# Kernel optimization log

Hardware: AMD Instinct MI355X
Metric: run time of the kernel (lower is better)

## Reference

```python
import jax, jax.numpy as jnp
import numpy as np

C = 32
KSHAPE = (C, C, 3, 3)  # (C_out, C_in, kH, kW)
BN_EPS = 1e-5


def _binary_act(x):
    # forward: sign(x); backward: identity clipped to |x|<1 (STE)
    xc = jnp.clip(x, -1.0, 1.0)
    return jax.lax.stop_gradient(jnp.sign(x) - xc) + xc


def _binarize_weight(w_flat, shape):
    w = w_flat.reshape(shape)
    scale = jax.lax.stop_gradient(jnp.mean(jnp.abs(w)))  # global scalar scale, detached
    wc = jnp.clip(w, -1.0, 1.0)
    # forward: scale*sign(w); backward flows through clamp(w,-1,1)
    return jax.lax.stop_gradient(scale * jnp.sign(w) - wc) + wc


def _bi_conv_bn(x, w_flat, gamma, beta, stride):
    xb = _binary_act(x)
    w = _binarize_weight(w_flat, KSHAPE)
    y = jax.lax.conv_general_dilated(
        xb, w, window_strides=(stride, stride), padding=[(1, 1), (1, 1)],
        dimension_numbers=('NCHW', 'OIHW', 'NCHW'))
    # BatchNorm2d in training mode (batch stats, biased variance)
    m = jnp.mean(y, axis=(0, 2, 3), keepdims=True)
    v = jnp.mean((y - m) ** 2, axis=(0, 2, 3), keepdims=True)
    yhat = (y - m) * jax.lax.rsqrt(v + BN_EPS)
    return gamma.reshape(1, -1, 1, 1) * yhat + beta.reshape(1, -1, 1, 1)


def setup_inputs() -> dict:
    key = jax.random.key(0)
    k1, k2, k3 = jax.random.split(key, 3)
    return {
        'x': jax.random.normal(k1, (32, C, 160, 160), dtype=jnp.float32),
        'w1': jax.random.normal(k2, (C * C * 9, 1), dtype=jnp.float32) * 0.05,
        'gamma1': jnp.ones((C,), dtype=jnp.float32),
        'beta1': jnp.zeros((C,), dtype=jnp.float32),
        'w2': jax.random.normal(k3, (C * C * 9, 1), dtype=jnp.float32) * 0.05,
        'gamma2': jnp.ones((C,), dtype=jnp.float32),
        'beta2': jnp.zeros((C,), dtype=jnp.float32),
    }


def reference(x, w1, gamma1, beta1, w2, gamma2, beta2):
    # bireal residual block, stride=1 => skip_op is Identity
    inner = _bi_conv_bn(x, w1, gamma1, beta1, 1) + x
    out = _bi_conv_bn(inner, w2, gamma2, beta2, 1) + inner
    return out
```

## Files before the change

### kernel.cpp

```cpp
#include <hip/hip_runtime.h>
#include <stdint.h>

#define NIMG 32
#define CH 32
#define HH 160
#define WW 160
#define HWL (HH*WW)
#define PRS 164
#define PHH 162
#define PIMG (PHH*PRS)
#define NPIX (NIMG*HWL)
#define HALO_WORDS 968

#define OFF_P     0
#define OFF_P2    3400704
#define OFF_INNER (OFF_P2 + 3400704)
#define OFF_WP    (OFF_INNER + 52428800)
#define OFF_CORR  (OFF_WP + 2304)
#define OFF_SC    (OFF_CORR + 2304)
#define OFF_SB    (OFF_SC + 128)

struct StatLine {
  int s1; int pad0; unsigned long long s2; char pad[112];
};

__device__ __forceinline__ unsigned short f2bf(float f) {
  unsigned u = __float_as_uint(f);
  u += 0x7fffu + ((u >> 16) & 1u);
  return (unsigned short)(u >> 16);
}
__device__ __forceinline__ float bf2f(unsigned short u) {
  return __uint_as_float((uint32_t)u << 16);
}

__device__ __forceinline__ void conv4(const uint32_t r[3][6], const uint32_t* wsh,
                                      int co, int& a0, int& a1, int& a2, int& a3)
{
  a0 = a1 = a2 = a3 = 0;
  #pragma unroll
  for (int dy = 0; dy < 3; ++dy) {
    #pragma unroll
    for (int dx = 0; dx < 3; ++dx) {
      uint32_t wvv = wsh[co * 9 + dy * 3 + dx];
      a0 += __popc(r[dy][0 + dx] ^ wvv);
      a1 += __popc(r[dy][1 + dx] ^ wvv);
      a2 += __popc(r[dy][2 + dx] ^ wvv);
      a3 += __popc(r[dy][3 + dx] ^ wvv);
    }
  }
}

__global__ __launch_bounds__(256, 2) void pack_prep(const float* __restrict__ x,
    const float* __restrict__ w1, const float* __restrict__ w2,
    uint32_t* __restrict__ P, uint32_t* __restrict__ P2, uint32_t* __restrict__ WP,
    int* __restrict__ CORR, float* __restrict__ SC, StatLine* __restrict__ SB)
{
  __shared__ float red[256];
  const int tid = threadIdx.x;
  const int b = blockIdx.x;

  if (b >= 1600) {
    if (b == 1842) {
      int* z = (int*)SB;
      for (int i = tid; i < 2048; i += 256) z[i] = 0;
      for (int cv = 0; cv < 2; ++cv) {
        const float* w = cv ? w2 : w1;
        float s = 0.f;
        for (int i = tid; i < 9216; i += 256) s += fabsf(w[i]);
        red[tid] = s;
        __syncthreads();
        for (int st = 128; st > 0; st >>= 1) {
          if (tid < st) red[tid] += red[tid + st];
          __syncthreads();
        }
        if (tid == 0) SC[cv] = red[0] / 9216.0f;
        for (int i = tid; i < 288; i += 256) {
          int co = i / 9, t = i - co * 9;
          uint32_t bw = 0;
          for (int ci = 0; ci < 32; ++ci)
            bw |= (w[(co * 32 + ci) * 9 + t] > 0.0f) ? (1u << ci) : 0u;
          WP[cv * 288 + i] = bw;
        }
        __syncthreads();
        for (int i = tid; i < 288; i += 256) {
          int cls = i / 32, co = i - cls * 32;
          int hc = cls / 3, wc = cls - hc * 3;
          int corr = 0;
          for (int t = 0; t < 9; ++t) {
            int dy = t / 3 - 1, dx = t % 3 - 1;
            bool inval = (hc == 0 && dy == -1) || (hc == 2 && dy == 1) ||
                         (wc == 0 && dx == -1) || (wc == 2 && dx == 1);
            if (inval) corr += 32 - 2 * __popc(WP[cv * 288 + co * 9 + t]);
          }
          CORR[cv * 288 + cls * 32 + co] = corr;
        }
        __syncthreads();
      }
    } else {
      int k = (b - 1600) * 256 + tid;
      uint32_t* buf = (k < 32 * HALO_WORDS) ? P : P2;
      int j = k % (32 * HALO_WORDS);
      int img = j / HALO_WORDS;
      int r = j - img * HALO_WORDS;
      int pr, pc;
      if (r < 164)      { pr = 0;   pc = r; }
      else if (r < 328) { pr = 161; pc = r - 164; }
      else {
        int k2 = r - 328;
        pr = 1 + (k2 >> 2);
        int q = k2 & 3;
        pc = (q == 0) ? 0 : (160 + q);
      }
      buf[img * PIMG + pr * PRS + pc] = 0;
    }
    return;
  }

  int g = b * 256 + tid;
  int grp = g >> 2;
  int k = g & 3;
  int p0 = grp * 8;
  int n = p0 / HWL;
  int i = p0 - n * HWL;
  const float* xb = x + (size_t)n * CH * HWL + i + (size_t)(k * 8) * HWL;
  float4 a0 = *reinterpret_cast<const float4*>(xb + 0 * HWL);
  float4 b0 = *reinterpret_cast<const float4*>(xb + 0 * HWL + 4);
  float4 a1 = *reinterpret_cast<const float4*>(xb + 1 * HWL);
  float4 b1 = *reinterpret_cast<const float4*>(xb + 1 * HWL + 4);
  float4 a2 = *reinterpret_cast<const float4*>(xb + 2 * HWL);
  float4 b2 = *reinterpret_cast<const float4*>(xb + 2 * HWL + 4);
  float4 a3 = *reinterpret_cast<const float4*>(xb + 3 * HWL);
  float4 b3 = *reinterpret_cast<const float4*>(xb + 3 * HWL + 4);
  float4 a4 = *reinterpret_cast<const float4*>(xb + 4 * HWL);
  float4 b4 = *reinterpret_cast<const float4*>(xb + 4 * HWL + 4);
  float4 a5 = *reinterpret_cast<const float4*>(xb + 5 * HWL);
  float4 b5 = *reinterpret_cast<const float4*>(xb + 5 * HWL + 4);
  float4 a6 = *reinterpret_cast<const float4*>(xb + 6 * HWL);
  float4 b6 = *reinterpret_cast<const float4*>(xb + 6 * HWL + 4);
  float4 a7 = *reinterpret_cast<const float4*>(xb + 7 * HWL);
  float4 b7 = *reinterpret_cast<const float4*>(xb + 7 * HWL + 4);

  uint32_t q0 = 0, q1 = 0, q2 = 0, q3 = 0, q4 = 0, q5 = 0, q6 = 0, q7 = 0;
  int c0 = k * 8;
  #define ACC(j, aj, bj)                                        \
    { uint32_t m = 1u << (c0 + j);                              \
      if (aj.x > 0.f) q0 |= m; if (aj.y > 0.f) q1 |= m;         \
      if (aj.z > 0.f) q2 |= m; if (aj.w > 0.f) q3 |= m;         \
      if (bj.x > 0.f) q4 |= m; if (bj.y > 0.f) q5 |= m;         \
      if (bj.z > 0.f) q6 |= m; if (bj.w > 0.f) q7 |= m; }
  ACC(0, a0, b0) ACC(1, a1, b1) ACC(2, a2, b2) ACC(3, a3, b3)
  ACC(4, a4, b4) ACC(5, a5, b5) ACC(6, a6, b6) ACC(7, a7, b7)
  #undef ACC

  q0 |= __shfl_xor(q0, 1); q1 |= __shfl_xor(q1, 1);
  q2 |= __shfl_xor(q2, 1); q3 |= __shfl_xor(q3, 1);
  q4 |= __shfl_xor(q4, 1); q5 |= __shfl_xor(q5, 1);
  q6 |= __shfl_xor(q6, 1); q7 |= __shfl_xor(q7, 1);
  q0 |= __shfl_xor(q0, 2); q1 |= __shfl_xor(q1, 2);
  q2 |= __shfl_xor(q2, 2); q3 |= __shfl_xor(q3, 2);
  q4 |= __shfl_xor(q4, 2); q5 |= __shfl_xor(q5, 2);
  q6 |= __shfl_xor(q6, 2); q7 |= __shfl_xor(q7, 2);

  int h = i / WW, w = i - (i / WW) * WW;
  uint32_t* pw = P + n * PIMG + (h + 1) * PRS + (w + 1);
  uint32_t wa = (k == 0) ? q0 : (k == 1) ? q1 : (k == 2) ? q2 : q3;
  uint32_t wb = (k == 0) ? q4 : (k == 1) ? q5 : (k == 2) ? q6 : q7;
  pw[k] = wa;
  pw[k + 4] = wb;
}

__global__ __launch_bounds__(256) void conv_stats(const uint32_t* __restrict__ P,
    const uint32_t* __restrict__ WP, const int* __restrict__ CORR,
    StatLine* __restrict__ sb)
{
  __shared__ uint32_t wsh[288];
  __shared__ int csh[288];
  __shared__ int ls1[32], ls2[32];
  const int tid = threadIdx.x;
  for (int i = tid; i < 288; i += 256) { wsh[i] = WP[i]; csh[i] = CORR[i]; }
  if (tid < 32) { ls1[tid] = 0; ls2[tid] = 0; }
  __syncthreads();

  int g = blockIdx.x * 256 + tid;
  int w4 = g % 40;
  int t1 = g / 40;
  int h = t1 % 160;
  int n = t1 / 160;

  const uint32_t* base = P + n * PIMG + h * PRS + w4 * 4;
  uint32_t r[3][6];
  #pragma unroll
  for (int dy = 0; dy < 3; ++dy) {
    uint4 a = *reinterpret_cast<const uint4*>(base + dy * PRS);
    uint2 bw = *reinterpret_cast<const uint2*>(base + dy * PRS + 4);
    r[dy][0] = a.x; r[dy][1] = a.y; r[dy][2] = a.z; r[dy][3] = a.w;
    r[dy][4] = bw.x; r[dy][5] = bw.y;
  }

  int rowc = (h == 0) ? 0 : ((h == 159) ? 6 : 3);
  int cls0  = rowc + ((w4 == 0) ? 0 : 1);
  int cls12 = rowc + 1;
  int cls3  = rowc + ((w4 == 39) ? 2 : 1);
  int lane = tid & 63;

  #pragma unroll
  for (int co = 0; co < 32; ++co) {
    int a0, a1, a2, a3;
    conv4(r, wsh, co, a0, a1, a2, a3);
    int d0 = 288 - 2 * a0 - csh[cls0 * 32 + co];
    int d1 = 288 - 2 * a1 - csh[cls12 * 32 + co];
    int d2 = 288 - 2 * a2 - csh[cls12 * 32 + co];
    int d3 = 288 - 2 * a3 - csh[cls3 * 32 + co];
    int ds = d0 + d1 + d2 + d3;
    int sq = d0 * d0 + d1 * d1 + d2 * d2 + d3 * d3;
    #pragma unroll
    for (int off = 32; off > 0; off >>= 1) {
      ds += __shfl_down(ds, off);
      sq += __shfl_down(sq, off);
    }
    if (lane == 0) { atomicAdd(&ls1[co], ds); atomicAdd(&ls2[co], sq); }
  }
  __syncthreads();
  if (tid < 32) {
    atomicAdd(&sb[tid].s1, ls1[tid]);
    atomicAdd(&sb[tid].s2, (unsigned long long)(long long)ls2[tid]);
  }
}

__global__ __launch_bounds__(256, 2) void conv_bn1(const uint32_t* __restrict__ P,
    const uint32_t* __restrict__ WP, const int* __restrict__ CORR,
    const float* __restrict__ x, const float* __restrict__ SCp,
    const StatLine* __restrict__ sb, const float* __restrict__ gamma,
    const float* __restrict__ beta, unsigned short* __restrict__ INNER,
    uint32_t* __restrict__ P2)
{
  __shared__ uint32_t wsh[288];
  __shared__ int csh[288];
  __shared__ float Ash[32], Bsh[32];
  const int tid = threadIdx.x;
  for (int i = tid; i < 288; i += 256) { wsh[i] = WP[i]; csh[i] = CORR[i]; }
  if (tid < 32) {
    double sc = (double)SCp[0];
    double m  = sc * (double)sb[tid].s1 / (double)NPIX;
    double ms = sc * sc * (double)(long long)sb[tid].s2 / (double)NPIX;
    float inv = (float)(1.0 / sqrt(ms - m * m + 1e-5));
    float gm = gamma[tid];
    Ash[tid] = gm * inv * (float)sc;
    Bsh[tid] = beta[tid] - gm * inv * (float)m;
  }
  __syncthreads();

  int g = blockIdx.x * 256 + tid;
  int w4 = g % 40;
  int t1 = g / 40;
  int h = t1 % 160;
  int n = t1 / 160;

  const uint32_t* base = P + n * PIMG + h * PRS + w4 * 4;
  uint32_t r[3][6];
  #pragma unroll
  for (int dy = 0; dy < 3; ++dy) {
    uint4 a = *reinterpret_cast<const uint4*>(base + dy * PRS);
    uint2 bw = *reinterpret_cast<const uint2*>(base + dy * PRS + 4);
    r[dy][0] = a.x; r[dy][1] = a.y; r[dy][2] = a.z; r[dy][3] = a.w;
    r[dy][4] = bw.x; r[dy][5] = bw.y;
  }
  int rowc = (h == 0) ? 0 : ((h == 159) ? 6 : 3);
  int cls0  = rowc + ((w4 == 0) ? 0 : 1);
  int cls12 = rowc + 1;
  int cls3  = rowc + ((w4 == 39) ? 2 : 1);

  int i = h * WW + w4 * 4;
  size_t pbase = (size_t)n * CH * HWL + i;

  float4 xv[32];
  #pragma unroll
  for (int j = 0; j < 32; ++j)
    xv[j] = *reinterpret_cast<const float4*>(x + pbase + (size_t)j * HWL);

  uint32_t bb0 = 0, bb1 = 0, bb2 = 0, bb3 = 0;
  #pragma unroll
  for (int co = 0; co < 32; ++co) {
    int a0, a1, a2, a3;
    conv4(r, wsh, co, a0, a1, a2, a3);
    int d0 = 288 - 2 * a0 - csh[cls0 * 32 + co];
    int d1 = 288 - 2 * a1 - csh[cls12 * 32 + co];
    int d2 = 288 - 2 * a2 - csh[cls12 * 32 + co];
    int d3 = 288 - 2 * a3 - csh[cls3 * 32 + co];
    float A = Ash[co], Bv = Bsh[co];
    float v0 = fmaf(A, (float)d0, Bv) + xv[co].x;
    float v1 = fmaf(A, (float)d1, Bv) + xv[co].y;
    float v2 = fmaf(A, (float)d2, Bv) + xv[co].z;
    float v3 = fmaf(A, (float)d3, Bv) + xv[co].w;
    ushort4 o; o.x = f2bf(v0); o.y = f2bf(v1); o.z = f2bf(v2); o.w = f2bf(v3);
    *reinterpret_cast<ushort4*>(INNER + pbase + (size_t)co * HWL) = o;
    uint32_t m = 1u << co;
    if (v0 > 0.f) bb0 |= m;
    if (v1 > 0.f) bb1 |= m;
    if (v2 > 0.f) bb2 |= m;
    if (v3 > 0.f) bb3 |= m;
  }
  uint32_t* pw = P2 + n * PIMG + (h + 1) * PRS + (w4 * 4 + 1);
  pw[0] = bb0; pw[1] = bb1; pw[2] = bb2; pw[3] = bb3;
}

__global__ __launch_bounds__(256, 2) void conv_bn2(const uint32_t* __restrict__ P2,
    const uint32_t* __restrict__ WP, const int* __restrict__ CORR,
    const unsigned short* __restrict__ INNER, const float* __restrict__ SCp,
    const StatLine* __restrict__ sb, const float* __restrict__ gamma,
    const float* __restrict__ beta, float* __restrict__ out)
{
  __shared__ uint32_t wsh[288];
  __shared__ int csh[288];
  __shared__ float Ash[32], Bsh[32];
  const int tid = threadIdx.x;
  for (int i = tid; i < 288; i += 256) { wsh[i] = WP[i]; csh[i] = CORR[i]; }
  if (tid < 32) {
    double sc = (double)SCp[0];
    double m  = sc * (double)sb[tid].s1 / (double)NPIX;
    double ms = sc * sc * (double)(long long)sb[tid].s2 / (double)NPIX;
    float inv = (float)(1.0 / sqrt(ms - m * m + 1e-5));
    float gm = gamma[tid];
    Ash[tid] = gm * inv * (float)sc;
    Bsh[tid] = beta[tid] - gm * inv * (float)m;
  }
  __syncthreads();

  int g = blockIdx.x * 256 + tid;
  int w4 = g % 40;
  int t1 = g / 40;
  int h = t1 % 160;
  int n = t1 / 160;

  const uint32_t* base = P2 + n * PIMG + h * PRS + w4 * 4;
  uint32_t r[3][6];
  #pragma unroll
  for (int dy = 0; dy < 3; ++dy) {
    uint4 a = *reinterpret_cast<const uint4*>(base + dy * PRS);
    uint2 bw = *reinterpret_cast<const uint2*>(base + dy * PRS + 4);
    r[dy][0] = a.x; r[dy][1] = a.y; r[dy][2] = a.z; r[dy][3] = a.w;
    r[dy][4] = bw.x; r[dy][5] = bw.y;
  }
  int rowc = (h == 0) ? 0 : ((h == 159) ? 6 : 3);
  int cls0  = rowc + ((w4 == 0) ? 0 : 1);
  int cls12 = rowc + 1;
  int cls3  = rowc + ((w4 == 39) ? 2 : 1);

  int i = h * WW + w4 * 4;
  size_t pbase = (size_t)n * CH * HWL + i;

  ushort4 iv[32];
  #pragma unroll
  for (int j = 0; j < 32; ++j)
    iv[j] = *reinterpret_cast<const ushort4*>(INNER + pbase + (size_t)j * HWL);

  #pragma unroll
  for (int co = 0; co < 32; ++co) {
    int a0, a1, a2, a3;
    conv4(r, wsh, co, a0, a1, a2, a3);
    int d0 = 288 - 2 * a0 - csh[cls0 * 32 + co];
    int d1 = 288 - 2 * a1 - csh[cls12 * 32 + co];
    int d2 = 288 - 2 * a2 - csh[cls12 * 32 + co];
    int d3 = 288 - 2 * a3 - csh[cls3 * 32 + co];
    float A = Ash[co], Bv = Bsh[co];
    float4 o;
    o.x = fmaf(A, (float)d0, Bv) + bf2f(iv[co].x);
    o.y = fmaf(A, (float)d1, Bv) + bf2f(iv[co].y);
    o.z = fmaf(A, (float)d2, Bv) + bf2f(iv[co].z);
    o.w = fmaf(A, (float)d3, Bv) + bf2f(iv[co].w);
    *reinterpret_cast<float4*>(out + pbase + (size_t)co * HWL) = o;
  }
}

extern "C" void kernel_launch(void* const* d_in, const int* in_sizes, int n_in,
                              void* d_out, int out_size, void* d_ws, size_t ws_size,
                              hipStream_t stream)
{
  (void)in_sizes; (void)n_in; (void)out_size; (void)ws_size;
  const float* x  = (const float*)d_in[0];
  const float* w1 = (const float*)d_in[1];
  const float* g1 = (const float*)d_in[2];
  const float* b1 = (const float*)d_in[3];
  const float* w2 = (const float*)d_in[4];
  const float* g2 = (const float*)d_in[5];
  const float* b2 = (const float*)d_in[6];
  float* out = (float*)d_out;
  char* ws = (char*)d_ws;

  uint32_t*       P     = (uint32_t*)(ws + OFF_P);
  uint32_t*       P2    = (uint32_t*)(ws + OFF_P2);
  unsigned short* INNER = (unsigned short*)(ws + OFF_INNER);
  uint32_t*       WP    = (uint32_t*)(ws + OFF_WP);
  int*            CORR  = (int*)(ws + OFF_CORR);
  float*          SC    = (float*)(ws + OFF_SC);
  StatLine*       SB    = (StatLine*)(ws + OFF_SB);

  pack_prep<<<1843, 256, 0, stream>>>(x, w1, w2, P, P2, WP, CORR, SC, SB);
  conv_stats<<<800, 256, 0, stream>>>(P, WP, CORR, SB);
  conv_bn1<<<800, 256, 0, stream>>>(P, WP, CORR, x, SC, SB, g1, b1, INNER, P2);
  conv_stats<<<800, 256, 0, stream>>>(P2, WP + 288, CORR + 288, SB + 32);
  conv_bn2<<<800, 256, 0, stream>>>(P2, WP + 288, CORR + 288, INNER, SC + 1, SB + 32, g2, b2, out);
}
```

Measured before the change: 205.0 us.

## Stage input tiles into LDS via global_load_lds DMA for sign packing

```diff
diff --git a/kernel.cpp b/kernel.cpp
--- a/kernel.cpp
+++ b/kernel.cpp
@@ -24,6 +24,12 @@
   int s1; int pad0; unsigned long long s2; char pad[112];
 };
 
+#define AS1 __attribute__((address_space(1)))
+#define AS3 __attribute__((address_space(3)))
+__device__ __forceinline__ void dma16(const float* g, float* l) {
+  __builtin_amdgcn_global_load_lds((const AS1 void*)g, (AS3 void*)l, 16, 0, 0);
+}
+
 __device__ __forceinline__ unsigned short f2bf(float f) {
   unsigned u = __float_as_uint(f);
   u += 0x7fffu + ((u >> 16) & 1u);
@@ -50,12 +56,12 @@
   }
 }
 
-__global__ __launch_bounds__(256, 2) void pack_prep(const float* __restrict__ x,
+__global__ __launch_bounds__(256) void pack_prep(const float* __restrict__ x,
     const float* __restrict__ w1, const float* __restrict__ w2,
     uint32_t* __restrict__ P, uint32_t* __restrict__ P2, uint32_t* __restrict__ WP,
     int* __restrict__ CORR, float* __restrict__ SC, StatLine* __restrict__ SB)
 {
-  __shared__ float red[256];
+  __shared__ float lds[16384];
   const int tid = threadIdx.x;
   const int b = blockIdx.x;
 
@@ -63,10 +69,18 @@
     if (b == 1842) {
       int* z = (int*)SB;
       for (int i = tid; i < 2048; i += 256) z[i] = 0;
+      float* wl  = lds;
+      float* red = lds + 9216;
+      uint32_t* wpl = (uint32_t*)(lds + 9600);
       for (int cv = 0; cv < 2; ++cv) {
         const float* w = cv ? w2 : w1;
         float s = 0.f;
-        for (int i = tid; i < 9216; i += 256) s += fabsf(w[i]);
+        #pragma unroll
+        for (int j = 0; j < 9; ++j) {
+          float4 v = *reinterpret_cast<const float4*>(w + (j * 256 + tid) * 4);
+          *reinterpret_cast<float4*>(wl + (j * 256 + tid) * 4) = v;
+          s += fabsf(v.x) + fabsf(v.y) + fabsf(v.z) + fabsf(v.w);
+        }
         red[tid] = s;
         __syncthreads();
         for (int st = 128; st > 0; st >>= 1) {
@@ -78,8 +92,9 @@
           int co = i / 9, t = i - co * 9;
           uint32_t bw = 0;
           for (int ci = 0; ci < 32; ++ci)
-            bw |= (w[(co * 32 + ci) * 9 + t] > 0.0f) ? (1u << ci) : 0u;
+            bw |= (wl[(co * 32 + ci) * 9 + t] > 0.0f) ? (1u << ci) : 0u;
           WP[cv * 288 + i] = bw;
+          wpl[i] = bw;
         }
         __syncthreads();
         for (int i = tid; i < 288; i += 256) {
@@ -90,7 +105,7 @@
             int dy = t / 3 - 1, dx = t % 3 - 1;
             bool inval = (hc == 0 && dy == -1) || (hc == 2 && dy == 1) ||
                          (wc == 0 && dx == -1) || (wc == 2 && dx == 1);
-            if (inval) corr += 32 - 2 * __popc(WP[cv * 288 + co * 9 + t]);
+            if (inval) corr += 32 - 2 * __popc(wpl[co * 9 + t]);
           }
           CORR[cv * 288 + cls * 32 + co] = corr;
         }
@@ -116,57 +131,30 @@
     return;
   }
 
-  int g = b * 256 + tid;
-  int grp = g >> 2;
-  int k = g & 3;
-  int p0 = grp * 8;
-  int n = p0 / HWL;
-  int i = p0 - n * HWL;
-  const float* xb = x + (size_t)n * CH * HWL + i + (size_t)(k * 8) * HWL;
-  float4 a0 = *reinterpret_cast<const float4*>(xb + 0 * HWL);
-  float4 b0 = *reinterpret_cast<const float4*>(xb + 0 * HWL + 4);
-  float4 a1 = *reinterpret_cast<const float4*>(xb + 1 * HWL);
-  float4 b1 = *reinterpret_cast<const float4*>(xb + 1 * HWL + 4);
-  float4 a2 = *reinterpret_cast<const float4*>(xb + 2 * HWL);
-  float4 b2 = *reinterpret_cast<const float4*>(xb + 2 * HWL + 4);
-  float4 a3 = *reinterpret_cast<const float4*>(xb + 3 * HWL);
-  float4 b3 = *reinterpret_cast<const float4*>(xb + 3 * HWL + 4);
-  float4 a4 = *reinterpret_cast<const float4*>(xb + 4 * HWL);
-  float4 b4 = *reinterpret_cast<const float4*>(xb + 4 * HWL + 4);
-  float4 a5 = *reinterpret_cast<const float4*>(xb + 5 * HWL);
-  float4 b5 = *reinterpret_cast<const float4*>(xb + 5 * HWL + 4);
-  float4 a6 = *reinterpret_cast<const float4*>(xb + 6 * HWL);
-  float4 b6 = *reinterpret_cast<const float4*>(xb + 6 * HWL + 4);
-  float4 a7 = *reinterpret_cast<const float4*>(xb + 7 * HWL);
-  float4 b7 = *reinterpret_cast<const float4*>(xb + 7 * HWL + 4);
-
-  uint32_t q0 = 0, q1 = 0, q2 = 0, q3 = 0, q4 = 0, q5 = 0, q6 = 0, q7 = 0;
-  int c0 = k * 8;
-  #define ACC(j, aj, bj)                                        \
-    { uint32_t m = 1u << (c0 + j);                              \
-      if (aj.x > 0.f) q0 |= m; if (aj.y > 0.f) q1 |= m;         \
-      if (aj.z > 0.f) q2 |= m; if (aj.w > 0.f) q3 |= m;         \
-      if (bj.x > 0.f) q4 |= m; if (bj.y > 0.f) q5 |= m;         \
-      if (bj.z > 0.f) q6 |= m; if (bj.w > 0.f) q7 |= m; }
-  ACC(0, a0, b0) ACC(1, a1, b1) ACC(2, a2, b2) ACC(3, a3, b3)
-  ACC(4, a4, b4) ACC(5, a5, b5) ACC(6, a6, b6) ACC(7, a7, b7)
-  #undef ACC
-
-  q0 |= __shfl_xor(q0, 1); q1 |= __shfl_xor(q1, 1);
-  q2 |= __shfl_xor(q2, 1); q3 |= __shfl_xor(q3, 1);
-  q4 |= __shfl_xor(q4, 1); q5 |= __shfl_xor(q5, 1);
-  q6 |= __shfl_xor(q6, 1); q7 |= __shfl_xor(q7, 1);
-  q0 |= __shfl_xor(q0, 2); q1 |= __shfl_xor(q1, 2);
-  q2 |= __shfl_xor(q2, 2); q3 |= __shfl_xor(q3, 2);
-  q4 |= __shfl_xor(q4, 2); q5 |= __shfl_xor(q5, 2);
-  q6 |= __shfl_xor(q6, 2); q7 |= __shfl_xor(q7, 2);
-
-  int h = i / WW, w = i - (i / WW) * WW;
+  int n = b / 50;
+  int p0 = (b - n * 50) * 512;
+  const float* xb = x + (size_t)n * CH * HWL + p0;
+  #pragma unroll
+  for (int it = 0; it < 16; ++it) {
+    int c = it * 2 + (tid >> 7);
+    const float* g = xb + (size_t)c * HWL + (tid & 127) * 4;
+    float* l = lds + it * 1024 + (tid >> 6) * 256;
+    dma16(g, l);
+  }
+  __syncthreads();
+
+  const float2* l2 = (const float2*)lds;
+  uint32_t b0 = 0, b1 = 0;
+  #pragma unroll
+  for (int c = 0; c < 32; ++c) {
+    float2 v = l2[c * 256 + tid];
+    if (v.x > 0.f) b0 |= 1u << c;
+    if (v.y > 0.f) b1 |= 1u << c;
+  }
+  int pxg = p0 + tid * 2;
+  int h = pxg / WW, w = pxg - h * WW;
   uint32_t* pw = P + n * PIMG + (h + 1) * PRS + (w + 1);
-  uint32_t wa = (k == 0) ? q0 : (k == 1) ? q1 : (k == 2) ? q2 : q3;
-  uint32_t wb = (k == 0) ? q4 : (k == 1) ? q5 : (k == 2) ? q6 : q7;
-  pw[k] = wa;
-  pw[k + 4] = wb;
+  pw[0] = b0; pw[1] = b1;
 }
 
 __global__ __launch_bounds__(256) void conv_stats(const uint32_t* __restrict__ P,
```

Result: faster. 174.6 us (-14.9%).
